# Performance work log

Measured on AMD Instinct MI355X. Metric: run time of the kernel, lower is better.

Reference implementation:

```python
import jax, jax.numpy as jnp
import numpy as np

K = 1024      # size_codebook
D = 64        # dim_codebook
N = 131072    # number of input vectors
GAMMA = 0.99
ALPHA = 1e-09
BETA = 0.25


def setup_inputs() -> dict:
    key = jax.random.key(0)
    k1, k2, k3 = jax.random.split(key, 3)
    X = jax.random.normal(k1, (N, D), dtype=jnp.float32)
    E = jax.random.normal(k2, (K, D), dtype=jnp.float32)
    cluster_sizes = jnp.zeros((K,), dtype=jnp.float32)
    moving_avg = E  # buffer initialized to a clone of E.weight
    return {"X": X, "E": E, "cluster_sizes": cluster_sizes, "moving_avg": moving_avg}


def reference(X, E, cluster_sizes, moving_avg):
    # squared euclidean distances: [N, K]
    X_sqnorm = jnp.sum(X * X, axis=1, keepdims=True)          # [N, 1]
    E_sqnorm = jnp.sum(E * E, axis=1)[None, :]                # [1, K]
    dist = X_sqnorm + E_sqnorm - 2.0 * (X @ E.T)              # [N, K]
    min_dist = jnp.min(dist, axis=1)                          # [N]
    argmins = jnp.argmin(dist, axis=1)                        # [N]
    Z_embs_raw = E[argmins]                                   # [N, D]

    # commitment loss (codebook is detached in the EMA variant)
    diff = X - jax.lax.stop_gradient(Z_embs_raw)
    loss = BETA * jnp.mean(jnp.sum(diff * diff, axis=1))

    # EMA codebook update (training mode, no-grad in torch)
    counts = jax.ops.segment_sum(jnp.ones((N,), dtype=X.dtype), argmins, num_segments=K)
    cs = GAMMA * cluster_sizes + (1.0 - GAMMA) * counts
    cs = (cs + ALPHA) / (1.0 + ALPHA * K / jnp.sum(cs))
    sums = jax.ops.segment_sum(X, argmins, num_segments=K)    # one_hot.T @ X, [K, D]
    ma = GAMMA * moving_avg + (1.0 - GAMMA) * sums
    E_new = ma / cs[:, None]

    # straight-through estimator
    Z_embs = X + jax.lax.stop_gradient(Z_embs_raw - X)
    return (Z_embs, loss, argmins, min_dist, E_new, cs, ma)
```

## Files before the change

kernel.cpp:

```cpp
#include <hip/hip_runtime.h>
#include <math.h>

#define NN 131072
#define KK 1024
#define DD 64
#define GAMMA 0.99f
#define ALPHA 1e-9f
#define BETA 0.25f

typedef float f32x4 __attribute__((ext_vector_type(4)));
typedef short bf16x8 __attribute__((ext_vector_type(8)));

__device__ __constant__ float OMG = (float)(1.0 - 0.99);

__device__ __forceinline__ void split_bf16(float v, unsigned short& h, unsigned short& l) {
    unsigned int b = __float_as_uint(v);
    unsigned int hb = b & 0xFFFF0000u;
    h = (unsigned short)(hb >> 16);
    float r = v - __uint_as_float(hb);
    unsigned int lb = __float_as_uint(r);
    lb += 0x7FFFu + ((lb >> 16) & 1u);
    l = (unsigned short)(lb >> 16);
}

__global__ __launch_bounds__(64)
void vq_prep(const float* __restrict__ E, float4* __restrict__ Efrag,
             float* __restrict__ esqh) {
    int nt = blockIdx.x;
    int l = threadIdx.x;
    int n = nt * 16 + (l & 15);
    int kb = (l >> 4) * 8;
    float ss = 0.f;
    #pragma unroll
    for (int ks = 0; ks < 2; ++ks) {
        const float4* xp = (const float4*)(E + (size_t)n * DD + ks * 32 + kb);
        float4 a = xp[0], b = xp[1];
        float v[8] = {a.x, a.y, a.z, a.w, b.x, b.y, b.z, b.w};
        union { float4 f; unsigned short u[8]; } H, L;
        #pragma unroll
        for (int j = 0; j < 8; ++j) {
            unsigned short hh, ll;
            split_bf16(v[j], hh, ll);
            H.u[j] = hh; L.u[j] = ll;
            ss = fmaf(v[j], v[j], ss);
        }
        int fid = nt * 4 + ks * 2;
        Efrag[(size_t)(fid + 0) * 64 + l] = H.f;
        Efrag[(size_t)(fid + 1) * 64 + l] = L.f;
    }
    ss += __shfl_xor(ss, 16, 64);
    ss += __shfl_xor(ss, 32, 64);
    if (l < 16) esqh[nt * 16 + l] = -0.5f * ss;
}

#define BM 64

__global__ __launch_bounds__(256, 2)
void vq_main(const float* __restrict__ X, const float* __restrict__ E,
             const float4* __restrict__ Efrag, const float* __restrict__ esqh,
             float* __restrict__ argf, float* __restrict__ mind,
             float* __restrict__ Z, int* __restrict__ cursor,
             int* __restrict__ rowlist, float* __restrict__ sumsFB,
             float* __restrict__ loss_part, int cap) {
    __shared__ float redv[128];
    __shared__ int redi[128];
    __shared__ int bidx[64];
    __shared__ float bsc[64];
    __shared__ float xsqs[64];
    __shared__ int fbflag[64];

    int tid = threadIdx.x;
    int lane = tid & 63, w = tid >> 6;
    int rg = w & 1, cg = w >> 1;
    int lc = lane & 15, lq = lane >> 4;

    size_t bb = (size_t)blockIdx.x * BM;
    size_t R0 = bb + rg * 32;

    bf16x8 ah[2][2], al[2][2];
    #pragma unroll
    for (int mt = 0; mt < 2; ++mt) {
        float xq = 0.f;
        #pragma unroll
        for (int ks = 0; ks < 2; ++ks) {
            const float4* xp =
                (const float4*)(X + (R0 + mt * 16 + lc) * DD + ks * 32 + lq * 8);
            float4 x0 = xp[0], x1 = xp[1];
            float v[8] = {x0.x, x0.y, x0.z, x0.w, x1.x, x1.y, x1.z, x1.w};
            union { bf16x8 s; unsigned short u[8]; } H, L;
            #pragma unroll
            for (int j = 0; j < 8; ++j) {
                unsigned short hh, ll;
                split_bf16(v[j], hh, ll);
                H.u[j] = hh; L.u[j] = ll;
                xq = fmaf(v[j], v[j], xq);
            }
            ah[mt][ks] = H.s;
            al[mt][ks] = L.s;
        }
        xq += __shfl_xor(xq, 16, 64);
        xq += __shfl_xor(xq, 32, 64);
        if (lane < 16) xsqs[rg * 32 + mt * 16 + lane] = xq;
    }

    float bestv[2][4];
    int besti[2][4];
    #pragma unroll
    for (int mt = 0; mt < 2; ++mt)
        #pragma unroll
        for (int r = 0; r < 4; ++r) { bestv[mt][r] = -3.402823466e38f; besti[mt][r] = 0; }

    const float4* bp = Efrag + (size_t)(cg * 32) * 256 + lane;
    const float* ep = esqh + cg * 512 + lc;

    float4 nb0 = bp[0], nb1 = bp[64], nb2 = bp[128], nb3 = bp[192];
    float en = ep[0];

    for (int nt = 0; nt < 32; ++nt) {
        float4 cb0 = nb0, cb1 = nb1, cb2 = nb2, cb3 = nb3;
        float ec = en;
        if (nt < 31) {
            const float4* q = bp + (size_t)(nt + 1) * 256;
            nb0 = q[0]; nb1 = q[64]; nb2 = q[128]; nb3 = q[192];
            en = ep[(nt + 1) * 16];
        }
        union { float4 f; bf16x8 s; } u0, u1, u2, u3;
        u0.f = cb0; u1.f = cb1; u2.f = cb2; u3.f = cb3;
        bf16x8 bh0 = u0.s, bl0 = u1.s, bh1 = u2.s, bl1 = u3.s;

        f32x4 acc[2];
        #pragma unroll
        for (int mt = 0; mt < 2; ++mt) acc[mt] = (f32x4){ec, ec, ec, ec};

        #pragma unroll
        for (int mt = 0; mt < 2; ++mt)
            acc[mt] = __builtin_amdgcn_mfma_f32_16x16x32_bf16(ah[mt][0], bh0, acc[mt], 0, 0, 0);
        #pragma unroll
        for (int mt = 0; mt < 2; ++mt)
            acc[mt] = __builtin_amdgcn_mfma_f32_16x16x32_bf16(ah[mt][1], bh1, acc[mt], 0, 0, 0);
        #pragma unroll
        for (int mt = 0; mt < 2; ++mt)
            acc[mt] = __builtin_amdgcn_mfma_f32_16x16x32_bf16(ah[mt][0], bl0, acc[mt], 0, 0, 0);
        #pragma unroll
        for (int mt = 0; mt < 2; ++mt)
            acc[mt] = __builtin_amdgcn_mfma_f32_16x16x32_bf16(ah[mt][1], bl1, acc[mt], 0, 0, 0);
        #pragma unroll
        for (int mt = 0; mt < 2; ++mt)
            acc[mt] = __builtin_amdgcn_mfma_f32_16x16x32_bf16(al[mt][0], bh0, acc[mt], 0, 0, 0);
        #pragma unroll
        for (int mt = 0; mt < 2; ++mt)
            acc[mt] = __builtin_amdgcn_mfma_f32_16x16x32_bf16(al[mt][1], bh1, acc[mt], 0, 0, 0);

        int n = cg * 512 + nt * 16 + lc;
        #pragma unroll
        for (int mt = 0; mt < 2; ++mt) {
            #pragma unroll
            for (int r = 0; r < 4; ++r) {
                float sc = acc[mt][r];
                if (sc > bestv[mt][r]) { bestv[mt][r] = sc; besti[mt][r] = n; }
            }
        }
    }

    #pragma unroll
    for (int off = 1; off <= 8; off <<= 1) {
        #pragma unroll
        for (int mt = 0; mt < 2; ++mt) {
            #pragma unroll
            for (int r = 0; r < 4; ++r) {
                float ov = __shfl_xor(bestv[mt][r], off, 64);
                int oi = __shfl_xor(besti[mt][r], off, 64);
                if (ov > bestv[mt][r] || (ov == bestv[mt][r] && oi < besti[mt][r])) {
                    bestv[mt][r] = ov; besti[mt][r] = oi;
                }
            }
        }
    }
    if (lc == 0) {
        #pragma unroll
        for (int mt = 0; mt < 2; ++mt)
            #pragma unroll
            for (int r = 0; r < 4; ++r) {
                int row = rg * 32 + mt * 16 + lq * 4 + r;
                redv[row * 2 + cg] = bestv[mt][r];
                redi[row * 2 + cg] = besti[mt][r];
            }
    }
    __syncthreads();
    if (tid < 64) {
        float v0 = redv[tid * 2], v1 = redv[tid * 2 + 1];
        int i0 = redi[tid * 2], i1 = redi[tid * 2 + 1];
        int pick = (v1 > v0 || (v1 == v0 && i1 < i0));
        bidx[tid] = pick ? i1 : i0;
        bsc[tid] = pick ? v1 : v0;
    }
    __syncthreads();

    if (tid < 64) {
        int row = tid;
        int bi = bidx[row];
        size_t grow = bb + row;
        float md = fmaf(-2.f, bsc[row], xsqs[row]);
        mind[grow] = md;
        argf[grow] = (float)bi;
        int pos = atomicAdd(&cursor[bi], 1);
        if (pos < cap) {
            rowlist[(size_t)bi * cap + pos] = (int)grow;
            fbflag[row] = 0;
        } else {
            fbflag[row] = 1;
        }
        #pragma unroll
        for (int m = 32; m; m >>= 1) md += __shfl_xor(md, m, 64);
        if (tid == 0) atomicAdd(&loss_part[blockIdx.x & 1023], md);
    }
    __syncthreads();

    #pragma unroll 4
    for (int it = 0; it < 16; ++it) {
        int row = w * 16 + it;
        int bi = bidx[row];
        size_t grow = bb + row;
        float e = E[(size_t)bi * DD + lane];
        Z[grow * DD + lane] = e;
        if (fbflag[row]) {
            float x = X[grow * DD + lane];
            atomicAdd(&sumsFB[(size_t)bi * DD + lane], x);
        }
    }
}

__global__ __launch_bounds__(256)
void vq_sum_ema(const float* __restrict__ X, const int* __restrict__ rowlist,
                const int* __restrict__ cursor, const float* __restrict__ sumsFB,
                const float* __restrict__ cluster_sizes,
                const float* __restrict__ loss_part, const float* __restrict__ mavg,
                float* __restrict__ o_ma, float* __restrict__ o_enew,
                float* __restrict__ o_cs, float* __restrict__ o_loss, int cap) {
    __shared__ float part[4][64];
    __shared__ float redt[4];
    int k = blockIdx.x;
    int lane = threadIdx.x & 63, w = threadIdx.x >> 6;

    float t = 0.f;
    for (int j = threadIdx.x; j < KK; j += 256)
        t += GAMMA * cluster_sizes[j] + OMG * (float)cursor[j];
    #pragma unroll
    for (int m = 32; m; m >>= 1) t += __shfl_xor(t, m, 64);
    if (lane == 0) redt[w] = t;
    __syncthreads();
    float total = redt[0] + redt[1] + redt[2] + redt[3];

    float csr = GAMMA * cluster_sizes[k] + OMG * (float)cursor[k];
    float cs = (csr + ALPHA) / (1.0f + (ALPHA * (float)KK) / total);
    if (threadIdx.x == 0) o_cs[k] = cs;

    if (k == 0) {
        float t2 = 0.f;
        for (int j = threadIdx.x; j < 1024; j += 256) t2 += loss_part[j];
        #pragma unroll
        for (int m = 32; m; m >>= 1) t2 += __shfl_xor(t2, m, 64);
        if (lane == 0) redt[w] = t2;
        __syncthreads();
        if (threadIdx.x == 0) {
            float l = redt[0] + redt[1] + redt[2] + redt[3];
            o_loss[0] = BETA * (l / (float)NN);
        }
    }

    int cnt = cursor[k];
    int nr = cnt < cap ? cnt : cap;
    const int* rl = rowlist + (size_t)k * cap;
    float acc = 0.f;
    #pragma unroll 4
    for (int i = w; i < nr; i += 4) {
        int r = rl[i];
        acc += X[(size_t)r * DD + lane];
    }
    part[w][lane] = acc;
    __syncthreads();
    if (w == 0) {
        float s = part[0][lane] + part[1][lane] + part[2][lane] + part[3][lane]
                + sumsFB[(size_t)k * DD + lane];
        float ma = GAMMA * mavg[(size_t)k * DD + lane] + OMG * s;
        o_ma[(size_t)k * DD + lane] = ma;
        o_enew[(size_t)k * DD + lane] = ma / cs;
    }
}

extern "C" void kernel_launch(void* const* d_in, const int* in_sizes, int n_in,
                              void* d_out, int out_size, void* d_ws, size_t ws_size,
                              hipStream_t stream) {
    const float* X = (const float*)d_in[0];
    const float* E = (const float*)d_in[1];
    const float* cluster_sizes = (const float*)d_in[2];
    const float* moving_avg = (const float*)d_in[3];

    float* out = (float*)d_out;
    float* o_Z = out;
    float* o_loss = o_Z + (size_t)NN * DD;
    float* o_arg = o_loss + 1;
    float* o_mind = o_arg + NN;
    float* o_enew = o_mind + NN;
    float* o_cs = o_enew + (size_t)KK * DD;
    float* o_ma = o_cs + KK;

    int* cursor = (int*)d_ws;
    float* loss_part = (float*)d_ws + 1024;
    float* sumsFB = loss_part + 1024;
    float* esqh = sumsFB + (size_t)KK * DD;
    float4* Efrag = (float4*)(esqh + KK);
    int* rowlist = (int*)(esqh + KK + (size_t)KK * DD);

    size_t base_bytes = (size_t)(1024 + 1024 + KK * DD + KK + KK * DD) * 4;
    long cap_l = ((long)ws_size - (long)base_bytes) / (long)(KK * sizeof(int));
    int cap = cap_l < 0 ? 0 : (cap_l > 1024 ? 1024 : (int)cap_l);

    hipMemsetAsync(d_ws, 0, (size_t)(1024 + 1024 + KK * DD) * 4, stream);

    vq_prep<<<KK / 16, 64, 0, stream>>>(E, Efrag, esqh);
    vq_main<<<NN / BM, 256, 0, stream>>>(X, E, Efrag, esqh, o_arg, o_mind, o_Z,
                                         cursor, rowlist, sumsFB, loss_part, cap);
    vq_sum_ema<<<KK, 256, 0, stream>>>(X, rowlist, cursor, sumsFB, cluster_sizes,
                                       loss_part, moving_avg, o_ma, o_enew,
                                       o_cs, o_loss, cap);
}
```

Before: 230.2 us.

## Stagger codebook tile order per block, double prefetch, widen EMA reduction blocks

The main distance loop now starts each block at a different codebook tile, offset by block index. This spreads the L2 and cache traffic on Efrag across tiles. The loop is also unrolled by two, with two independent prefetch buffers, so loads sit further ahead of the MFMA work. The segment-sum/EMA kernel moves from 256 to 1024 threads per cluster, giving more parallel row gathers per codebook entry, at the cost of heavier reductions and lower occupancy per CU.

```diff
diff --git a/kernel.cpp b/kernel.cpp
--- a/kernel.cpp
+++ b/kernel.cpp
@@ -113,52 +113,99 @@
     const float4* bp = Efrag + (size_t)(cg * 32) * 256 + lane;
     const float* ep = esqh + cg * 512 + lc;
 
-    float4 nb0 = bp[0], nb1 = bp[64], nb2 = bp[128], nb3 = bp[192];
-    float en = ep[0];
-
-    for (int nt = 0; nt < 32; ++nt) {
-        float4 cb0 = nb0, cb1 = nb1, cb2 = nb2, cb3 = nb3;
-        float ec = en;
-        if (nt < 31) {
-            const float4* q = bp + (size_t)(nt + 1) * 256;
-            nb0 = q[0]; nb1 = q[64]; nb2 = q[128]; nb3 = q[192];
-            en = ep[(nt + 1) * 16];
-        }
-        union { float4 f; bf16x8 s; } u0, u1, u2, u3;
-        u0.f = cb0; u1.f = cb1; u2.f = cb2; u3.f = cb3;
-        bf16x8 bh0 = u0.s, bl0 = u1.s, bh1 = u2.s, bl1 = u3.s;
-
-        f32x4 acc[2];
-        #pragma unroll
-        for (int mt = 0; mt < 2; ++mt) acc[mt] = (f32x4){ec, ec, ec, ec};
-
-        #pragma unroll
-        for (int mt = 0; mt < 2; ++mt)
-            acc[mt] = __builtin_amdgcn_mfma_f32_16x16x32_bf16(ah[mt][0], bh0, acc[mt], 0, 0, 0);
-        #pragma unroll
-        for (int mt = 0; mt < 2; ++mt)
-            acc[mt] = __builtin_amdgcn_mfma_f32_16x16x32_bf16(ah[mt][1], bh1, acc[mt], 0, 0, 0);
-        #pragma unroll
-        for (int mt = 0; mt < 2; ++mt)
-            acc[mt] = __builtin_amdgcn_mfma_f32_16x16x32_bf16(ah[mt][0], bl0, acc[mt], 0, 0, 0);
-        #pragma unroll
-        for (int mt = 0; mt < 2; ++mt)
-            acc[mt] = __builtin_amdgcn_mfma_f32_16x16x32_bf16(ah[mt][1], bl1, acc[mt], 0, 0, 0);
-        #pragma unroll
-        for (int mt = 0; mt < 2; ++mt)
-            acc[mt] = __builtin_amdgcn_mfma_f32_16x16x32_bf16(al[mt][0], bh0, acc[mt], 0, 0, 0);
-        #pragma unroll
-        for (int mt = 0; mt < 2; ++mt)
-            acc[mt] = __builtin_amdgcn_mfma_f32_16x16x32_bf16(al[mt][1], bh1, acc[mt], 0, 0, 0);
-
-        int n = cg * 512 + nt * 16 + lc;
-        #pragma unroll
-        for (int mt = 0; mt < 2; ++mt) {
-            #pragma unroll
-            for (int r = 0; r < 4; ++r) {
-                float sc = acc[mt][r];
-                if (sc > bestv[mt][r]) { bestv[mt][r] = sc; besti[mt][r] = n; }
-            }
+    int st = (blockIdx.x >> 3) & 31;
+
+    int p0 = st;
+    int p1 = (st + 1) & 31;
+    const float4* q0 = bp + (size_t)p0 * 256;
+    const float4* q1 = bp + (size_t)p1 * 256;
+    float4 na0 = q0[0], na1 = q0[64], na2 = q0[128], na3 = q0[192];
+    float ea = ep[p0 * 16];
+    float4 mb0 = q1[0], mb1 = q1[64], mb2 = q1[128], mb3 = q1[192];
+    float eb = ep[p1 * 16];
+
+    for (int i = 0; i < 32; i += 2) {
+        {
+            int ntp = (i + st) & 31;
+            union { float4 f; bf16x8 s; } u0, u1, u2, u3;
+            u0.f = na0; u1.f = na1; u2.f = na2; u3.f = na3;
+            float ec = ea;
+            if (i + 2 < 32) {
+                int np = (i + 2 + st) & 31;
+                const float4* q = bp + (size_t)np * 256;
+                na0 = q[0]; na1 = q[64]; na2 = q[128]; na3 = q[192];
+                ea = ep[np * 16];
+            }
+            f32x4 acc[2];
+            #pragma unroll
+            for (int mt = 0; mt < 2; ++mt) acc[mt] = (f32x4){ec, ec, ec, ec};
+            #pragma unroll
+            for (int mt = 0; mt < 2; ++mt)
+                acc[mt] = __builtin_amdgcn_mfma_f32_16x16x32_bf16(ah[mt][0], u0.s, acc[mt], 0, 0, 0);
+            #pragma unroll
+            for (int mt = 0; mt < 2; ++mt)
+                acc[mt] = __builtin_amdgcn_mfma_f32_16x16x32_bf16(ah[mt][1], u2.s, acc[mt], 0, 0, 0);
+            #pragma unroll
+            for (int mt = 0; mt < 2; ++mt)
+                acc[mt] = __builtin_amdgcn_mfma_f32_16x16x32_bf16(ah[mt][0], u1.s, acc[mt], 0, 0, 0);
+            #pragma unroll
+            for (int mt = 0; mt < 2; ++mt)
+                acc[mt] = __builtin_amdgcn_mfma_f32_16x16x32_bf16(ah[mt][1], u3.s, acc[mt], 0, 0, 0);
+            #pragma unroll
+            for (int mt = 0; mt < 2; ++mt)
+                acc[mt] = __builtin_amdgcn_mfma_f32_16x16x32_bf16(al[mt][0], u0.s, acc[mt], 0, 0, 0);
+            #pragma unroll
+            for (int mt = 0; mt < 2; ++mt)
+                acc[mt] = __builtin_amdgcn_mfma_f32_16x16x32_bf16(al[mt][1], u2.s, acc[mt], 0, 0, 0);
+            int n = cg * 512 + ntp * 16 + lc;
+            #pragma unroll
+            for (int mt = 0; mt < 2; ++mt)
+                #pragma unroll
+                for (int r = 0; r < 4; ++r) {
+                    float sc = acc[mt][r];
+                    if (sc > bestv[mt][r]) { bestv[mt][r] = sc; besti[mt][r] = n; }
+                }
+        }
+        {
+            int ntp = (i + 1 + st) & 31;
+            union { float4 f; bf16x8 s; } u0, u1, u2, u3;
+            u0.f = mb0; u1.f = mb1; u2.f = mb2; u3.f = mb3;
+            float ec = eb;
+            if (i + 3 < 32) {
+                int np = (i + 3 + st) & 31;
+                const float4* q = bp + (size_t)np * 256;
+                mb0 = q[0]; mb1 = q[64]; mb2 = q[128]; mb3 = q[192];
+                eb = ep[np * 16];
+            }
+            f32x4 acc[2];
+            #pragma unroll
+            for (int mt = 0; mt < 2; ++mt) acc[mt] = (f32x4){ec, ec, ec, ec};
+            #pragma unroll
+            for (int mt = 0; mt < 2; ++mt)
+                acc[mt] = __builtin_amdgcn_mfma_f32_16x16x32_bf16(ah[mt][0], u0.s, acc[mt], 0, 0, 0);
+            #pragma unroll
+            for (int mt = 0; mt < 2; ++mt)
+                acc[mt] = __builtin_amdgcn_mfma_f32_16x16x32_bf16(ah[mt][1], u2.s, acc[mt], 0, 0, 0);
+            #pragma unroll
+            for (int mt = 0; mt < 2; ++mt)
+                acc[mt] = __builtin_amdgcn_mfma_f32_16x16x32_bf16(ah[mt][0], u1.s, acc[mt], 0, 0, 0);
+            #pragma unroll
+            for (int mt = 0; mt < 2; ++mt)
+                acc[mt] = __builtin_amdgcn_mfma_f32_16x16x32_bf16(ah[mt][1], u3.s, acc[mt], 0, 0, 0);
+            #pragma unroll
+            for (int mt = 0; mt < 2; ++mt)
+                acc[mt] = __builtin_amdgcn_mfma_f32_16x16x32_bf16(al[mt][0], u0.s, acc[mt], 0, 0, 0);
+            #pragma unroll
+            for (int mt = 0; mt < 2; ++mt)
+                acc[mt] = __builtin_amdgcn_mfma_f32_16x16x32_bf16(al[mt][1], u2.s, acc[mt], 0, 0, 0);
+            int n = cg * 512 + ntp * 16 + lc;
+            #pragma unroll
+            for (int mt = 0; mt < 2; ++mt)
+                #pragma unroll
+                for (int r = 0; r < 4; ++r) {
+                    float sc = acc[mt][r];
+                    if (sc > bestv[mt][r]) { bestv[mt][r] = sc; besti[mt][r] = n; }
+                }
         }
     }
 
@@ -230,40 +277,42 @@
     }
 }
 
-__global__ __launch_bounds__(256)
+__global__ __launch_bounds__(1024)
 void vq_sum_ema(const float* __restrict__ X, const int* __restrict__ rowlist,
                 const int* __restrict__ cursor, const float* __restrict__ sumsFB,
                 const float* __restrict__ cluster_sizes,
                 const float* __restrict__ loss_part, const float* __restrict__ mavg,
                 float* __restrict__ o_ma, float* __restrict__ o_enew,
                 float* __restrict__ o_cs, float* __restrict__ o_loss, int cap) {
-    __shared__ float part[4][64];
-    __shared__ float redt[4];
+    __shared__ float part[16][64];
+    __shared__ float redt[16];
     int k = blockIdx.x;
     int lane = threadIdx.x & 63, w = threadIdx.x >> 6;
 
-    float t = 0.f;
-    for (int j = threadIdx.x; j < KK; j += 256)
-        t += GAMMA * cluster_sizes[j] + OMG * (float)cursor[j];
+    float t = GAMMA * cluster_sizes[threadIdx.x] + OMG * (float)cursor[threadIdx.x];
     #pragma unroll
     for (int m = 32; m; m >>= 1) t += __shfl_xor(t, m, 64);
     if (lane == 0) redt[w] = t;
     __syncthreads();
-    float total = redt[0] + redt[1] + redt[2] + redt[3];
+    float total = 0.f;
+    #pragma unroll
+    for (int j = 0; j < 16; ++j) total += redt[j];
 
     float csr = GAMMA * cluster_sizes[k] + OMG * (float)cursor[k];
     float cs = (csr + ALPHA) / (1.0f + (ALPHA * (float)KK) / total);
     if (threadIdx.x == 0) o_cs[k] = cs;
 
     if (k == 0) {
-        float t2 = 0.f;
-        for (int j = threadIdx.x; j < 1024; j += 256) t2 += loss_part[j];
+        __syncthreads();
+        float t2 = loss_part[threadIdx.x];
         #pragma unroll
         for (int m = 32; m; m >>= 1) t2 += __shfl_xor(t2, m, 64);
         if (lane == 0) redt[w] = t2;
         __syncthreads();
         if (threadIdx.x == 0) {
-            float l = redt[0] + redt[1] + redt[2] + redt[3];
+            float l = 0.f;
+            #pragma unroll
+            for (int j = 0; j < 16; ++j) l += redt[j];
             o_loss[0] = BETA * (l / (float)NN);
         }
     }
@@ -273,15 +322,16 @@
     const int* rl = rowlist + (size_t)k * cap;
     float acc = 0.f;
     #pragma unroll 4
-    for (int i = w; i < nr; i += 4) {
+    for (int i = w; i < nr; i += 16) {
         int r = rl[i];
         acc += X[(size_t)r * DD + lane];
     }
     part[w][lane] = acc;
     __syncthreads();
     if (w == 0) {
-        float s = part[0][lane] + part[1][lane] + part[2][lane] + part[3][lane]
-                + sumsFB[(size_t)k * DD + lane];
+        float s = sumsFB[(size_t)k * DD + lane];
+        #pragma unroll
+        for (int j = 0; j < 16; ++j) s += part[j][lane];
         float ma = GAMMA * mavg[(size_t)k * DD + lane] + OMG * s;
         o_ma[(size_t)k * DD + lane] = ma;
         o_enew[(size_t)k * DD + lane] = ma / cs;
@@ -321,7 +371,7 @@
     vq_prep<<<KK / 16, 64, 0, stream>>>(E, Efrag, esqh);
     vq_main<<<NN / BM, 256, 0, stream>>>(X, E, Efrag, esqh, o_arg, o_mind, o_Z,
                                          cursor, rowlist, sumsFB, loss_part, cap);
-    vq_sum_ema<<<KK, 256, 0, stream>>>(X, rowlist, cursor, sumsFB, cluster_sizes,
-                                       loss_part, moving_avg, o_ma, o_enew,
-                                       o_cs, o_loss, cap);
-}
+    vq_sum_ema<<<KK, 1024, 0, stream>>>(X, rowlist, cursor, sumsFB, cluster_sizes,
+                                        loss_part, moving_avg, o_ma, o_enew,
+                                        o_cs, o_loss, cap);
+}
```

Measured after the change: 206.6 us. 1.11x faster.

## Stage codebook fragments in LDS with double buffering and widen row tile

Applied to the files above, without the earlier changes.

The main kernel now covers 128 rows per block, with each wave owning 32 rows and sweeping the full codebook. Codebook fragments are staged cooperatively into a double-buffered LDS ring, so all four waves share each global load instead of every wave streaming its own half of the codebook. This removes the cross-wave argmin merge, but it adds about 36 KB of LDS per block and a barrier per chunk, which may limit occupancy. The EMA kernel also moves to 1024 threads per block, giving more parallelism to the row gather and the reductions.

```diff
diff --git a/kernel.cpp b/kernel.cpp
--- a/kernel.cpp
+++ b/kernel.cpp
@@ -53,29 +53,30 @@
     if (l < 16) esqh[nt * 16 + l] = -0.5f * ss;
 }
 
-#define BM 64
-
-__global__ __launch_bounds__(256, 2)
+#define BM 128
+
+__global__ __launch_bounds__(256, 4)
 void vq_main(const float* __restrict__ X, const float* __restrict__ E,
              const float4* __restrict__ Efrag, const float* __restrict__ esqh,
              float* __restrict__ argf, float* __restrict__ mind,
              float* __restrict__ Z, int* __restrict__ cursor,
              int* __restrict__ rowlist, float* __restrict__ sumsFB,
              float* __restrict__ loss_part, int cap) {
-    __shared__ float redv[128];
-    __shared__ int redi[128];
-    __shared__ int bidx[64];
-    __shared__ float bsc[64];
-    __shared__ float xsqs[64];
-    __shared__ int fbflag[64];
+    __shared__ float4 buf[2][1024];
+    __shared__ float esql[KK];
+    __shared__ int bidx[BM];
+    __shared__ float bsc[BM];
+    __shared__ float xsqs[BM];
+    __shared__ int fbflag[BM];
 
     int tid = threadIdx.x;
     int lane = tid & 63, w = tid >> 6;
-    int rg = w & 1, cg = w >> 1;
     int lc = lane & 15, lq = lane >> 4;
 
     size_t bb = (size_t)blockIdx.x * BM;
-    size_t R0 = bb + rg * 32;
+    size_t R0 = bb + w * 32;
+
+    ((float4*)esql)[tid] = ((const float4*)esqh)[tid];
 
     bf16x8 ah[2][2], al[2][2];
     #pragma unroll
@@ -100,7 +101,7 @@
         }
         xq += __shfl_xor(xq, 16, 64);
         xq += __shfl_xor(xq, 32, 64);
-        if (lane < 16) xsqs[rg * 32 + mt * 16 + lane] = xq;
+        if (lane < 16) xsqs[w * 32 + mt * 16 + lane] = xq;
     }
 
     float bestv[2][4];
@@ -110,55 +111,56 @@
         #pragma unroll
         for (int r = 0; r < 4; ++r) { bestv[mt][r] = -3.402823466e38f; besti[mt][r] = 0; }
 
-    const float4* bp = Efrag + (size_t)(cg * 32) * 256 + lane;
-    const float* ep = esqh + cg * 512 + lc;
-
-    float4 nb0 = bp[0], nb1 = bp[64], nb2 = bp[128], nb3 = bp[192];
-    float en = ep[0];
-
-    for (int nt = 0; nt < 32; ++nt) {
-        float4 cb0 = nb0, cb1 = nb1, cb2 = nb2, cb3 = nb3;
-        float ec = en;
-        if (nt < 31) {
-            const float4* q = bp + (size_t)(nt + 1) * 256;
-            nb0 = q[0]; nb1 = q[64]; nb2 = q[128]; nb3 = q[192];
-            en = ep[(nt + 1) * 16];
-        }
-        union { float4 f; bf16x8 s; } u0, u1, u2, u3;
-        u0.f = cb0; u1.f = cb1; u2.f = cb2; u3.f = cb3;
-        bf16x8 bh0 = u0.s, bl0 = u1.s, bh1 = u2.s, bl1 = u3.s;
-
-        f32x4 acc[2];
-        #pragma unroll
-        for (int mt = 0; mt < 2; ++mt) acc[mt] = (f32x4){ec, ec, ec, ec};
-
-        #pragma unroll
-        for (int mt = 0; mt < 2; ++mt)
-            acc[mt] = __builtin_amdgcn_mfma_f32_16x16x32_bf16(ah[mt][0], bh0, acc[mt], 0, 0, 0);
-        #pragma unroll
-        for (int mt = 0; mt < 2; ++mt)
-            acc[mt] = __builtin_amdgcn_mfma_f32_16x16x32_bf16(ah[mt][1], bh1, acc[mt], 0, 0, 0);
-        #pragma unroll
-        for (int mt = 0; mt < 2; ++mt)
-            acc[mt] = __builtin_amdgcn_mfma_f32_16x16x32_bf16(ah[mt][0], bl0, acc[mt], 0, 0, 0);
-        #pragma unroll
-        for (int mt = 0; mt < 2; ++mt)
-            acc[mt] = __builtin_amdgcn_mfma_f32_16x16x32_bf16(ah[mt][1], bl1, acc[mt], 0, 0, 0);
-        #pragma unroll
-        for (int mt = 0; mt < 2; ++mt)
-            acc[mt] = __builtin_amdgcn_mfma_f32_16x16x32_bf16(al[mt][0], bh0, acc[mt], 0, 0, 0);
-        #pragma unroll
-        for (int mt = 0; mt < 2; ++mt)
-            acc[mt] = __builtin_amdgcn_mfma_f32_16x16x32_bf16(al[mt][1], bh1, acc[mt], 0, 0, 0);
-
-        int n = cg * 512 + nt * 16 + lc;
-        #pragma unroll
-        for (int mt = 0; mt < 2; ++mt) {
+    float4 nxt[4];
+    #pragma unroll
+    for (int r = 0; r < 4; ++r) nxt[r] = Efrag[r * 256 + tid];
+    #pragma unroll
+    for (int r = 0; r < 4; ++r) buf[0][r * 256 + tid] = nxt[r];
+    __syncthreads();
+
+    for (int c = 0; c < 16; ++c) {
+        int pb = c & 1;
+        if (c + 1 < 16) {
+            #pragma unroll
+            for (int r = 0; r < 4; ++r)
+                nxt[r] = Efrag[(size_t)(c + 1) * 1024 + r * 256 + tid];
+        }
+        const float4* bc = buf[pb];
+        #pragma unroll
+        for (int t = 0; t < 4; ++t) {
+            int nt = c * 4 + t;
+            float ec = esql[nt * 16 + lc];
+            bf16x8 bh0 = *(const bf16x8*)&bc[t * 256 + 0 * 64 + lane];
+            bf16x8 bl0 = *(const bf16x8*)&bc[t * 256 + 1 * 64 + lane];
+            bf16x8 bh1 = *(const bf16x8*)&bc[t * 256 + 2 * 64 + lane];
+            bf16x8 bl1 = *(const bf16x8*)&bc[t * 256 + 3 * 64 + lane];
+
+            f32x4 a0 = (f32x4){ec, ec, ec, ec};
+            f32x4 a1 = (f32x4){ec, ec, ec, ec};
+            a0 = __builtin_amdgcn_mfma_f32_16x16x32_bf16(ah[0][0], bh0, a0, 0, 0, 0);
+            a1 = __builtin_amdgcn_mfma_f32_16x16x32_bf16(ah[1][0], bh0, a1, 0, 0, 0);
+            a0 = __builtin_amdgcn_mfma_f32_16x16x32_bf16(ah[0][1], bh1, a0, 0, 0, 0);
+            a1 = __builtin_amdgcn_mfma_f32_16x16x32_bf16(ah[1][1], bh1, a1, 0, 0, 0);
+            a0 = __builtin_amdgcn_mfma_f32_16x16x32_bf16(ah[0][0], bl0, a0, 0, 0, 0);
+            a1 = __builtin_amdgcn_mfma_f32_16x16x32_bf16(ah[1][0], bl0, a1, 0, 0, 0);
+            a0 = __builtin_amdgcn_mfma_f32_16x16x32_bf16(ah[0][1], bl1, a0, 0, 0, 0);
+            a1 = __builtin_amdgcn_mfma_f32_16x16x32_bf16(ah[1][1], bl1, a1, 0, 0, 0);
+            a0 = __builtin_amdgcn_mfma_f32_16x16x32_bf16(al[0][0], bh0, a0, 0, 0, 0);
+            a1 = __builtin_amdgcn_mfma_f32_16x16x32_bf16(al[1][0], bh0, a1, 0, 0, 0);
+            a0 = __builtin_amdgcn_mfma_f32_16x16x32_bf16(al[0][1], bh1, a0, 0, 0, 0);
+            a1 = __builtin_amdgcn_mfma_f32_16x16x32_bf16(al[1][1], bh1, a1, 0, 0, 0);
+
+            int n = nt * 16 + lc;
             #pragma unroll
             for (int r = 0; r < 4; ++r) {
-                float sc = acc[mt][r];
-                if (sc > bestv[mt][r]) { bestv[mt][r] = sc; besti[mt][r] = n; }
+                if (a0[r] > bestv[0][r]) { bestv[0][r] = a0[r]; besti[0][r] = n; }
+                if (a1[r] > bestv[1][r]) { bestv[1][r] = a1[r]; besti[1][r] = n; }
             }
+        }
+        if (c + 1 < 16) {
+            #pragma unroll
+            for (int r = 0; r < 4; ++r) buf[1 - pb][r * 256 + tid] = nxt[r];
+            __syncthreads();
         }
     }
 
@@ -181,22 +183,14 @@
         for (int mt = 0; mt < 2; ++mt)
             #pragma unroll
             for (int r = 0; r < 4; ++r) {
-                int row = rg * 32 + mt * 16 + lq * 4 + r;
-                redv[row * 2 + cg] = bestv[mt][r];
-                redi[row * 2 + cg] = besti[mt][r];
+                int row = w * 32 + mt * 16 + lq * 4 + r;
+                bidx[row] = besti[mt][r];
+                bsc[row] = bestv[mt][r];
             }
     }
     __syncthreads();
-    if (tid < 64) {
-        float v0 = redv[tid * 2], v1 = redv[tid * 2 + 1];
-        int i0 = redi[tid * 2], i1 = redi[tid * 2 + 1];
-        int pick = (v1 > v0 || (v1 == v0 && i1 < i0));
-        bidx[tid] = pick ? i1 : i0;
-        bsc[tid] = pick ? v1 : v0;
-    }
-    __syncthreads();
-
-    if (tid < 64) {
+
+    if (tid < 128) {
         int row = tid;
         int bi = bidx[row];
         size_t grow = bb + row;
@@ -212,13 +206,13 @@
         }
         #pragma unroll
         for (int m = 32; m; m >>= 1) md += __shfl_xor(md, m, 64);
-        if (tid == 0) atomicAdd(&loss_part[blockIdx.x & 1023], md);
+        if (lane == 0) atomicAdd(&loss_part[(blockIdx.x * 2 + w) & 1023], md);
     }
     __syncthreads();
 
     #pragma unroll 4
-    for (int it = 0; it < 16; ++it) {
-        int row = w * 16 + it;
+    for (int it = 0; it < 32; ++it) {
+        int row = w * 32 + it;
         int bi = bidx[row];
         size_t grow = bb + row;
         float e = E[(size_t)bi * DD + lane];
@@ -230,40 +224,42 @@
     }
 }
 
-__global__ __launch_bounds__(256)
+__global__ __launch_bounds__(1024)
 void vq_sum_ema(const float* __restrict__ X, const int* __restrict__ rowlist,
                 const int* __restrict__ cursor, const float* __restrict__ sumsFB,
                 const float* __restrict__ cluster_sizes,
                 const float* __restrict__ loss_part, const float* __restrict__ mavg,
                 float* __restrict__ o_ma, float* __restrict__ o_enew,
                 float* __restrict__ o_cs, float* __restrict__ o_loss, int cap) {
-    __shared__ float part[4][64];
-    __shared__ float redt[4];
+    __shared__ float part[16][64];
+    __shared__ float redt[16];
     int k = blockIdx.x;
     int lane = threadIdx.x & 63, w = threadIdx.x >> 6;
 
-    float t = 0.f;
-    for (int j = threadIdx.x; j < KK; j += 256)
-        t += GAMMA * cluster_sizes[j] + OMG * (float)cursor[j];
+    float t = GAMMA * cluster_sizes[threadIdx.x] + OMG * (float)cursor[threadIdx.x];
     #pragma unroll
     for (int m = 32; m; m >>= 1) t += __shfl_xor(t, m, 64);
     if (lane == 0) redt[w] = t;
     __syncthreads();
-    float total = redt[0] + redt[1] + redt[2] + redt[3];
+    float total = 0.f;
+    #pragma unroll
+    for (int j = 0; j < 16; ++j) total += redt[j];
 
     float csr = GAMMA * cluster_sizes[k] + OMG * (float)cursor[k];
     float cs = (csr + ALPHA) / (1.0f + (ALPHA * (float)KK) / total);
     if (threadIdx.x == 0) o_cs[k] = cs;
 
     if (k == 0) {
-        float t2 = 0.f;
-        for (int j = threadIdx.x; j < 1024; j += 256) t2 += loss_part[j];
+        __syncthreads();
+        float t2 = loss_part[threadIdx.x];
         #pragma unroll
         for (int m = 32; m; m >>= 1) t2 += __shfl_xor(t2, m, 64);
         if (lane == 0) redt[w] = t2;
         __syncthreads();
         if (threadIdx.x == 0) {
-            float l = redt[0] + redt[1] + redt[2] + redt[3];
+            float l = 0.f;
+            #pragma unroll
+            for (int j = 0; j < 16; ++j) l += redt[j];
             o_loss[0] = BETA * (l / (float)NN);
         }
     }
@@ -273,15 +269,16 @@
     const int* rl = rowlist + (size_t)k * cap;
     float acc = 0.f;
     #pragma unroll 4
-    for (int i = w; i < nr; i += 4) {
+    for (int i = w; i < nr; i += 16) {
         int r = rl[i];
         acc += X[(size_t)r * DD + lane];
     }
     part[w][lane] = acc;
     __syncthreads();
     if (w == 0) {
-        float s = part[0][lane] + part[1][lane] + part[2][lane] + part[3][lane]
-                + sumsFB[(size_t)k * DD + lane];
+        float s = sumsFB[(size_t)k * DD + lane];
+        #pragma unroll
+        for (int j = 0; j < 16; ++j) s += part[j][lane];
         float ma = GAMMA * mavg[(size_t)k * DD + lane] + OMG * s;
         o_ma[(size_t)k * DD + lane] = ma;
         o_enew[(size_t)k * DD + lane] = ma / cs;
@@ -321,7 +318,7 @@
     vq_prep<<<KK / 16, 64, 0, stream>>>(E, Efrag, esqh);
     vq_main<<<NN / BM, 256, 0, stream>>>(X, E, Efrag, esqh, o_arg, o_mind, o_Z,
                                          cursor, rowlist, sumsFB, loss_part, cap);
-    vq_sum_ema<<<KK, 256, 0, stream>>>(X, rowlist, cursor, sumsFB, cluster_sizes,
-                                       loss_part, moving_avg, o_ma, o_enew,
-                                       o_cs, o_loss, cap);
-}
+    vq_sum_ema<<<KK, 1024, 0, stream>>>(X, rowlist, cursor, sumsFB, cluster_sizes,
+                                        loss_part, moving_avg, o_ma, o_enew,
+                                        o_cs, o_loss, cap);
+}
```

After: 214.4 us. 1.07x faster.
